# Optimization experiments

Measured on AMD Instinct MI355X. Metric: run time of the kernel, lower is better.

## Reference

```python
import jax, jax.numpy as jnp
import numpy as np

D_MODEL = 1024
HIDDEN = 4096
N_EXPERTS = 8
TOP_K = 2


def setup_inputs() -> dict:
    key = jax.random.key(0)
    ks = jax.random.split(key, 7)
    x = jax.random.normal(ks[0], (4, 2048, D_MODEL), dtype=jnp.float32)
    s = 0.02
    Wg = jax.random.normal(ks[1], (D_MODEL, N_EXPERTS), dtype=jnp.float32) * s
    bg = jnp.zeros((N_EXPERTS,), dtype=jnp.float32)
    W1 = jax.random.normal(ks[2], (N_EXPERTS, D_MODEL, HIDDEN), dtype=jnp.float32) * s
    b1 = jnp.zeros((N_EXPERTS, HIDDEN), dtype=jnp.float32)
    W2 = jax.random.normal(ks[3], (N_EXPERTS, HIDDEN, D_MODEL), dtype=jnp.float32) * s
    b2 = jnp.zeros((N_EXPERTS, D_MODEL), dtype=jnp.float32)
    return {"x": x, "Wg": Wg, "bg": bg, "W1": W1, "b1": b1, "W2": W2, "b2": b2}


def reference(x, Wg, bg, W1, b1, W2, b2):
    B, T, D = x.shape
    xf = x.reshape(-1, D)                      # (N, D)
    N = xf.shape[0]

    # --- top-k gate ---
    logits = xf @ Wg + bg                      # (N, E)
    all_probs = jax.nn.softmax(logits, axis=-1)
    topk_logits, topk_idx = jax.lax.top_k(logits, TOP_K)   # (N, k)
    topk_gates = jax.nn.softmax(topk_logits, axis=-1)      # (N, k), sums to 1

    # scatter gates into dense (N, E) masks (matches torch scatter_add_)
    rows = jnp.arange(N)[:, None]
    gate_mask = jnp.zeros((N, N_EXPERTS), dtype=xf.dtype).at[rows, topk_idx].add(topk_gates)
    dispatch_mask = jnp.zeros((N, N_EXPERTS), dtype=xf.dtype).at[rows, topk_idx].add(1.0)

    # --- experts: dense batched form; unselected tokens have gate 0 so math matches ---
    h = jnp.einsum('nd,edh->neh', xf, W1) + b1             # (N, E, H)
    h = jax.nn.relu(h)
    y = jnp.einsum('neh,ehd->ned', h, W2) + b2             # (N, E, D)
    out = jnp.einsum('ned,ne->nd', y, gate_mask)           # weighted combine
    outputs = out.reshape(B, T, D)

    # --- load-balance loss + metadata ---
    tokens_per_expert = (dispatch_mask > 0).sum(axis=0)
    assignment_fraction = gate_mask.sum(axis=0) / N
    expected_prob = all_probs.mean(axis=0)
    load_balance_loss = (expected_prob * assignment_fraction).sum() * N_EXPERTS

    return (outputs, load_balance_loss, tokens_per_expert, expected_prob, assignment_fraction)
```

## Files before the change

### kernel.cpp

```cpp
#include <hip/hip_runtime.h>
#include <stdint.h>

#define D_MODEL 1024
#define HID     4096
#define NE      8
#define NTOK    8192
#define NSLOT   (NTOK*2)
#define TM      128
#define MAX_RB  136
#define MPAD    (MAX_RB*TM)
#define HHALF   2048
#define GATE_BLOCKS 32

typedef unsigned short u16;
typedef __attribute__((ext_vector_type(8))) __bf16 bf16x8;
typedef __attribute__((ext_vector_type(4))) float  f32x4;

__device__ __forceinline__ u16 f2bu(float f){
  uint32_t u = __builtin_bit_cast(uint32_t, f);
  uint32_t r = (u + 0x7FFFu + ((u >> 16) & 1u)) >> 16;
  return (u16)r;
}

__device__ __forceinline__ void gload16(const u16* src, u16* lds){
  __builtin_amdgcn_global_load_lds((const __attribute__((address_space(1))) void*)src,
                                   (__attribute__((address_space(3))) void*)lds, 16, 0, 0);
}

__device__ __forceinline__ int xcd_swz(int w, int nwg){
  int q = nwg >> 3;
  return (w & 7) * q + (w >> 3);
}

#define WAITV(n) do{ asm volatile("s_waitcnt vmcnt(" #n ")" ::: "memory"); \
                     __builtin_amdgcn_sched_barrier(0); }while(0)
#define BARX()   do{ __builtin_amdgcn_sched_barrier(0); \
                     __builtin_amdgcn_s_barrier(); \
                     __builtin_amdgcn_sched_barrier(0); }while(0)

__global__ __launch_bounds__(256) void xcvt_kernel(const float* __restrict__ x, u16* __restrict__ x16){
  size_t i = (size_t)blockIdx.x*256 + threadIdx.x;
  const float4* p = (const float4*)(x + i*8);
  float4 a = p[0], b = p[1];
  u16 o[8] = {f2bu(a.x),f2bu(a.y),f2bu(a.z),f2bu(a.w),f2bu(b.x),f2bu(b.y),f2bu(b.z),f2bu(b.w)};
  *(int4*)(x16 + i*8) = *(int4*)o;
}

__global__ __launch_bounds__(256) void transpose_cvt(const float* __restrict__ in,
                                                     u16* __restrict__ out, int R, int C)
{
  __shared__ float tile[32][33];
  int e = blockIdx.z;
  int r0 = blockIdx.y * 32, c0 = blockIdx.x * 32;
  const float* src = in + (size_t)e * R * C;
  u16* dst = out + (size_t)e * R * C;
  int tx = threadIdx.x, ty = threadIdx.y;
#pragma unroll
  for (int i = 0; i < 4; i++){
    int r = r0 + ty + i*8;
    tile[ty + i*8][tx] = src[(size_t)r * C + c0 + tx];
  }
  __syncthreads();
#pragma unroll
  for (int i = 0; i < 4; i++){
    int c = c0 + ty + i*8;
    dst[(size_t)c * R + r0 + tx] = f2bu(tile[tx][ty + i*8]);
  }
}

__global__ __launch_bounds__(256) void gate_kernel(
    const float* __restrict__ x, const float* __restrict__ Wg, const float* __restrict__ bg,
    int* __restrict__ topk, float* __restrict__ gates,
    float* __restrict__ part_probs, float* __restrict__ part_assign, int* __restrict__ part_cnt)
{
  __shared__ float sp[256][8];
  __shared__ float sa[256][8];
  __shared__ int   sc[256][8];
  int t = threadIdx.x;
  int n = blockIdx.x * 256 + t;
  float lg[8];
#pragma unroll
  for (int e = 0; e < 8; e++) lg[e] = bg[e];
  const float4* xr = (const float4*)(x + (size_t)n * D_MODEL);
  for (int j = 0; j < D_MODEL/4; j++){
    float4 v = xr[j];
    const float* wr = Wg + (size_t)j * 32;
#pragma unroll
    for (int e = 0; e < 8; e++)
      lg[e] += v.x*wr[e] + v.y*wr[8+e] + v.z*wr[16+e] + v.w*wr[24+e];
  }
  float m = lg[0];
#pragma unroll
  for (int e = 1; e < 8; e++) m = fmaxf(m, lg[e]);
  float p[8]; float s = 0.f;
#pragma unroll
  for (int e = 0; e < 8; e++){ p[e] = expf(lg[e]-m); s += p[e]; }
  float inv = 1.f / s;
  int bi = 0; float best = lg[0];
#pragma unroll
  for (int e = 1; e < 8; e++) if (lg[e] > best){ best = lg[e]; bi = e; }
  int bi2 = 0; float best2 = -3.0e38f;
#pragma unroll
  for (int e = 0; e < 8; e++) if (e != bi && lg[e] > best2){ best2 = lg[e]; bi2 = e; }
  float t1 = expf(best2 - best);
  float g0 = 1.f / (1.f + t1);
  float g1 = t1 / (1.f + t1);
  topk[2*n] = bi;  topk[2*n+1] = bi2;
  gates[2*n] = g0; gates[2*n+1] = g1;
#pragma unroll
  for (int e = 0; e < 8; e++){
    sp[t][e] = p[e] * inv;
    sa[t][e] = (e == bi) ? g0 : ((e == bi2) ? g1 : 0.f);
    sc[t][e] = (e == bi || e == bi2) ? 1 : 0;
  }
  __syncthreads();
  if (t < 8){
    float s2 = 0.f; for (int i = 0; i < 256; i++) s2 += sp[i][t];
    part_probs[blockIdx.x*8 + t] = s2;
  } else if (t < 16){
    int e = t - 8; float s2 = 0.f; for (int i = 0; i < 256; i++) s2 += sa[i][e];
    part_assign[blockIdx.x*8 + e] = s2;
  } else if (t < 24){
    int e = t - 16; int c = 0; for (int i = 0; i < 256; i++) c += sc[i][e];
    part_cnt[blockIdx.x*8 + e] = c;
  }
}

__global__ __launch_bounds__(256) void scan_kernel(const int* __restrict__ part_cnt,
                                                   int* __restrict__ counts,
                                                   int* __restrict__ padded_off,
                                                   int* __restrict__ cursor,
                                                   int* __restrict__ block_expert,
                                                   int* __restrict__ routed)
{
  __shared__ int off[NE+1];
  int t = threadIdx.x;
  if (t == 0){
    int o = 0; off[0] = 0;
    for (int e = 0; e < NE; e++){
      int c = 0;
      for (int b = 0; b < GATE_BLOCKS; b++) c += part_cnt[b*8 + e];
      counts[e] = c;
      o += ((c + TM - 1) / TM) * TM;
      off[e+1] = o;
    }
    for (int e = 0; e <= NE; e++) padded_off[e] = off[e];
  }
  __syncthreads();
  if (t < NE) cursor[t] = 0;
  for (int rb = t; rb < MAX_RB; rb += 256){
    int e = -1;
    int r = rb * TM;
    for (int j = 0; j < NE; j++)
      if (r >= off[j] && r < off[j+1]) e = j;
    block_expert[rb] = e;
  }
  for (int i = t; i < MPAD; i += 256) routed[i] = -1;
}

__global__ __launch_bounds__(256) void place_kernel(const int* __restrict__ topk,
                                                    const int* __restrict__ padded_off,
                                                    int* __restrict__ cursor,
                                                    int* __restrict__ routed)
{
  int s = blockIdx.x * 256 + threadIdx.x;
  int e = topk[s];
  int pos = padded_off[e] + atomicAdd(&cursor[e], 1);
  routed[pos] = s;
}

__global__ __launch_bounds__(256, 3) void gemm1_kernel(
    const u16* __restrict__ x16, const u16* __restrict__ w1t, const float* __restrict__ b1,
    const int* __restrict__ routed, const int* __restrict__ block_expert,
    u16* __restrict__ h, int half)
{
  int l = xcd_swz(blockIdx.x, gridDim.x);
  int rb = l >> 4, cb = l & 15;
  int e = block_expert[rb];
  if (e < 0) return;
  __shared__ __align__(16) u16 Al[3][128][32];
  __shared__ __align__(16) u16 Bl[3][128][32];
  u16* AF = &Al[0][0][0];
  u16* BF = &Bl[0][0][0];
  int t = threadIdx.x;
  int lane = t & 63, wid = t >> 6;

  int srow0 = wid*32 + (lane >> 2);
  int sch = (lane & 3) * 8;

  int slot0 = routed[rb*TM + srow0];
  int slot1 = routed[rb*TM + srow0 + 16];
  int tok0 = slot0 >= 0 ? (slot0 >> 1) : 0;
  int tok1 = slot1 >= 0 ? (slot1 >> 1) : 0;
  const u16* srcA0 = x16 + (size_t)tok0 * D_MODEL + sch;
  const u16* srcA1 = x16 + (size_t)tok1 * D_MODEL + sch;
  const u16* wb = w1t + ((size_t)e*HID + (size_t)half*HHALF + (size_t)cb*128) * D_MODEL + sch;
  const u16* srcB0 = wb + (size_t)srow0 * D_MODEL;
  const u16* srcB1 = wb + (size_t)(srow0 + 16) * D_MODEL;

  int wr = wid >> 1, wc = wid & 1;
  int fr = lane & 15, fk = lane >> 4;
  f32x4 acc[4][4];
#pragma unroll
  for (int i = 0; i < 4; i++)
#pragma unroll
    for (int j = 0; j < 4; j++) acc[i][j] = (f32x4){0.f,0.f,0.f,0.f};

#define STG1(bo, kk) do{ \
    gload16(srcA0 + (kk), AF + (bo) + wid*1024); \
    gload16(srcA1 + (kk), AF + (bo) + wid*1024 + 512); \
    gload16(srcB0 + (kk), BF + (bo) + wid*1024); \
    gload16(srcB1 + (kk), BF + (bo) + wid*1024 + 512); } while(0)

#define CMP1(bo) do{ \
    bf16x8 af[4], bf[4]; \
    _Pragma("unroll") \
    for (int mm = 0; mm < 4; mm++) af[mm] = *(const bf16x8*)(AF + (bo) + (wr*64 + mm*16 + fr)*32 + fk*8); \
    _Pragma("unroll") \
    for (int nn = 0; nn < 4; nn++) bf[nn] = *(const bf16x8*)(BF + (bo) + (wc*64 + nn*16 + fr)*32 + fk*8); \
    _Pragma("unroll") \
    for (int mm = 0; mm < 4; mm++) \
      _Pragma("unroll") \
      for (int nn = 0; nn < 4; nn++) \
        acc[mm][nn] = __builtin_amdgcn_mfma_f32_16x16x32_bf16(af[mm], bf[nn], acc[mm][nn], 0, 0, 0); } while(0)

  const int nk = D_MODEL/32;
  STG1(0, 0); STG1(4096, 32); STG1(8192, 64);
  int bo = 0;
  for (int i = 0; i < nk - 2; i++){
    WAITV(8);
    BARX();
    CMP1(bo);
    BARX();
    if (i < nk - 3) STG1(bo, (i+3)*32);
    bo = (bo == 8192) ? 0 : bo + 4096;
  }
  WAITV(4); BARX(); CMP1(bo); BARX();
  bo = (bo == 8192) ? 0 : bo + 4096;
  WAITV(0); BARX(); CMP1(bo);

  int r4 = fk * 4;
#pragma unroll
  for (int nn = 0; nn < 4; nn++){
    int ct = wc*64 + nn*16 + fr;
    float bias = b1[(size_t)e*HID + (size_t)half*HHALF + cb*128 + ct];
#pragma unroll
    for (int mm = 0; mm < 4; mm++){
#pragma unroll
      for (int r = 0; r < 4; r++){
        int rt = wr*64 + mm*16 + r4 + r;
        float v = acc[mm][nn][r] + bias;
        v = v > 0.f ? v : 0.f;
        h[(size_t)(rb*TM + rt) * HHALF + cb*128 + ct] = f2bu(v);
      }
    }
  }
#undef STG1
#undef CMP1
}

__global__ __launch_bounds__(256, 3) void gemm2_kernel(
    const u16* __restrict__ h, const u16* __restrict__ w2t,
    const int* __restrict__ routed, const int* __restrict__ block_expert,
    const float* __restrict__ gates, float* __restrict__ y, int half)
{
  int l = xcd_swz(blockIdx.x, gridDim.x);
  int rb = l >> 3, cb = l & 7;
  int e = block_expert[rb];
  if (e < 0) return;
  __shared__ __align__(16) u16 Al[3][128][32];
  __shared__ __align__(16) u16 Bl[3][128][32];
  __shared__ int   rslot[128];
  __shared__ float rgate[128];
  u16* AF = &Al[0][0][0];
  u16* BF = &Bl[0][0][0];
  int t = threadIdx.x;
  int lane = t & 63, wid = t >> 6;
  if (t < 128){
    int s = routed[rb*TM + t];
    rslot[t] = s;
    rgate[t] = (s >= 0) ? gates[s] : 0.f;
  }

  int srow0 = wid*32 + (lane >> 2);
  int sch = (lane & 3) * 8;
  const u16* srcA0 = h + (size_t)(rb*TM + srow0) * HHALF + sch;
  const u16* srcA1 = h + (size_t)(rb*TM + srow0 + 16) * HHALF + sch;
  const u16* wb = w2t + ((size_t)e*D_MODEL + (size_t)cb*128) * HID + (size_t)half*HHALF + sch;
  const u16* srcB0 = wb + (size_t)srow0 * HID;
  const u16* srcB1 = wb + (size_t)(srow0 + 16) * HID;

  int wr = wid >> 1, wc = wid & 1;
  int fr = lane & 15, fk = lane >> 4;
  f32x4 acc[4][4];
#pragma unroll
  for (int i = 0; i < 4; i++)
#pragma unroll
    for (int j = 0; j < 4; j++) acc[i][j] = (f32x4){0.f,0.f,0.f,0.f};

#define STG2(bo, kk) do{ \
    gload16(srcA0 + (kk), AF + (bo) + wid*1024); \
    gload16(srcA1 + (kk), AF + (bo) + wid*1024 + 512); \
    gload16(srcB0 + (kk), BF + (bo) + wid*1024); \
    gload16(srcB1 + (kk), BF + (bo) + wid*1024 + 512); } while(0)

#define CMP2(bo) do{ \
    bf16x8 af[4], bf[4]; \
    _Pragma("unroll") \
    for (int mm = 0; mm < 4; mm++) af[mm] = *(const bf16x8*)(AF + (bo) + (wr*64 + mm*16 + fr)*32 + fk*8); \
    _Pragma("unroll") \
    for (int nn = 0; nn < 4; nn++) bf[nn] = *(const bf16x8*)(BF + (bo) + (wc*64 + nn*16 + fr)*32 + fk*8); \
    _Pragma("unroll") \
    for (int mm = 0; mm < 4; mm++) \
      _Pragma("unroll") \
      for (int nn = 0; nn < 4; nn++) \
        acc[mm][nn] = __builtin_amdgcn_mfma_f32_16x16x32_bf16(af[mm], bf[nn], acc[mm][nn], 0, 0, 0); } while(0)

  const int nk = HHALF/32;
  STG2(0, 0); STG2(4096, 32); STG2(8192, 64);
  int bo = 0;
  for (int i = 0; i < nk - 2; i++){
    WAITV(8);
    BARX();
    CMP2(bo);
    BARX();
    if (i < nk - 3) STG2(bo, (i+3)*32);
    bo = (bo == 8192) ? 0 : bo + 4096;
  }
  WAITV(4); BARX(); CMP2(bo); BARX();
  bo = (bo == 8192) ? 0 : bo + 4096;
  WAITV(0); BARX(); CMP2(bo);

  int r4 = fk * 4;
#pragma unroll
  for (int mm = 0; mm < 4; mm++){
#pragma unroll
    for (int r = 0; r < 4; r++){
      int rt = wr*64 + mm*16 + r4 + r;
      int slot = rslot[rt];
      if (slot < 0) continue;
      float g = rgate[rt];
#pragma unroll
      for (int nn = 0; nn < 4; nn++){
        int ct = wc*64 + nn*16 + fr;
        size_t idx = (size_t)slot * D_MODEL + cb*128 + ct;
        float val = g * acc[mm][nn][r];
        if (half == 0) y[idx] = val;
        else           y[idx] += val;
      }
    }
  }
#undef STG2
#undef CMP2
}

__global__ __launch_bounds__(256) void combine_kernel(
    const float* __restrict__ y, const int* __restrict__ topk, const float* __restrict__ gates,
    const float* __restrict__ b2, float* __restrict__ out)
{
  int i = blockIdx.x * 256 + threadIdx.x;
  int n = i >> 8;
  int d = (i & 255) * 4;
  float4 a  = *(const float4*)(y + (size_t)(2*n)   * D_MODEL + d);
  float4 b  = *(const float4*)(y + (size_t)(2*n+1) * D_MODEL + d);
  int e0 = topk[2*n], e1 = topk[2*n+1];
  float g0 = gates[2*n], g1 = gates[2*n+1];
  float4 c0 = *(const float4*)(b2 + (size_t)e0 * D_MODEL + d);
  float4 c1 = *(const float4*)(b2 + (size_t)e1 * D_MODEL + d);
  float4 o;
  o.x = a.x + b.x + g0*c0.x + g1*c1.x;
  o.y = a.y + b.y + g0*c0.y + g1*c1.y;
  o.z = a.z + b.z + g0*c0.z + g1*c1.z;
  o.w = a.w + b.w + g0*c0.w + g1*c1.w;
  *(float4*)(out + (size_t)n * D_MODEL + d) = o;
}

__global__ void finalize_kernel(const float* __restrict__ part_probs,
                                const float* __restrict__ part_assign,
                                const int* __restrict__ counts,
                                float* __restrict__ out_tail)
{
  __shared__ float ep[8], af[8];
  int t = threadIdx.x;
  if (t < 8){
    float s = 0.f;
    for (int b = 0; b < GATE_BLOCKS; b++) s += part_probs[b*8 + t];
    ep[t] = s / (float)NTOK;
  } else if (t < 16){
    int e = t - 8; float s = 0.f;
    for (int b = 0; b < GATE_BLOCKS; b++) s += part_assign[b*8 + e];
    af[e] = s / (float)NTOK;
  }
  __syncthreads();
  if (t == 0){
    float loss = 0.f;
    for (int e = 0; e < 8; e++) loss += ep[e] * af[e];
    out_tail[0] = loss * (float)NE;
  }
  if (t < 8){
    out_tail[1 + t]  = (float)counts[t];
    out_tail[9 + t]  = ep[t];
    out_tail[17 + t] = af[t];
  }
}

extern "C" void kernel_launch(void* const* d_in, const int* in_sizes, int n_in,
                              void* d_out, int out_size, void* d_ws, size_t ws_size,
                              hipStream_t stream)
{
  const float* x  = (const float*)d_in[0];
  const float* Wg = (const float*)d_in[1];
  const float* bg = (const float*)d_in[2];
  const float* W1 = (const float*)d_in[3];
  const float* b1 = (const float*)d_in[4];
  const float* W2 = (const float*)d_in[5];
  const float* b2 = (const float*)d_in[6];
  float* out = (float*)d_out;

  char* ws = (char*)d_ws;
  size_t o = 0;
  auto alloc = [&](size_t bytes) -> char* {
    char* p = ws + o; o = (o + bytes + 255) & ~(size_t)255; return p;
  };
  int*   topk        = (int*)   alloc((size_t)NSLOT*4);
  float* gates       = (float*) alloc((size_t)NSLOT*4);
  int*   counts      = (int*)   alloc(NE*4);
  int*   padded_off  = (int*)   alloc((NE+1)*4);
  int*   cursor      = (int*)   alloc(NE*4);
  int*   block_exp   = (int*)   alloc(MAX_RB*4);
  int*   routed      = (int*)   alloc((size_t)MPAD*4);
  float* part_probs  = (float*) alloc(GATE_BLOCKS*8*4);
  float* part_assign = (float*) alloc(GATE_BLOCKS*8*4);
  int*   part_cnt    = (int*)   alloc(GATE_BLOCKS*8*4);
  u16*   x16         = (u16*)   alloc((size_t)NTOK*D_MODEL*2);
  u16*   w1t         = (u16*)   alloc((size_t)NE*HID*D_MODEL*2);
  u16*   w2t         = (u16*)   alloc((size_t)NE*HID*D_MODEL*2);
  u16*   hbuf        = (u16*)   alloc((size_t)MPAD*HHALF*2);
  float* ybuf        = (float*) alloc((size_t)NSLOT*D_MODEL*4);
  (void)ws_size; (void)in_sizes; (void)n_in; (void)out_size;

  transpose_cvt<<<dim3(HID/32, D_MODEL/32, NE), dim3(32,8), 0, stream>>>(W1, w1t, D_MODEL, HID);
  transpose_cvt<<<dim3(D_MODEL/32, HID/32, NE), dim3(32,8), 0, stream>>>(W2, w2t, HID, D_MODEL);
  xcvt_kernel<<<(NTOK*D_MODEL)/(256*8), 256, 0, stream>>>(x, x16);
  gate_kernel<<<GATE_BLOCKS, 256, 0, stream>>>(x, Wg, bg, topk, gates, part_probs, part_assign, part_cnt);
  scan_kernel<<<1, 256, 0, stream>>>(part_cnt, counts, padded_off, cursor, block_exp, routed);
  place_kernel<<<NSLOT/256, 256, 0, stream>>>(topk, padded_off, cursor, routed);
  for (int half = 0; half < 2; half++){
    gemm1_kernel<<<16*MAX_RB, 256, 0, stream>>>(x16, w1t, b1, routed, block_exp, hbuf, half);
    gemm2_kernel<<<8*MAX_RB, 256, 0, stream>>>(hbuf, w2t, routed, block_exp, gates, ybuf, half);
  }
  combine_kernel<<<NTOK, 256, 0, stream>>>(ybuf, topk, gates, b2, out);
  finalize_kernel<<<1, 64, 0, stream>>>(part_probs, part_assign, counts, out + (size_t)NTOK*D_MODEL);
}
```

Before: 688.4 us.

## Enlarge expert GEMM tiles to 256x256 with 512-thread blocks

Doubles the GEMM block tile from 128x128 to 256x256, uses 8 waves per block, and raises the routing row-block size to 256, so MAX_RB and the grid shapes change to match. Each wave now computes 128x64 and loads its A fragments one at a time. The aim is more data reuse per LDS load and less global traffic per flop. In exchange, the larger row blocks add more padding waste per expert, the grids are smaller with possible tail imbalance, and the bigger accumulators raise register pressure (launch bounds 512,2) with 96KB of LDS per block.

```diff
diff --git a/kernel.cpp b/kernel.cpp
--- a/kernel.cpp
+++ b/kernel.cpp
@@ -6,8 +6,8 @@
 #define NE      8
 #define NTOK    8192
 #define NSLOT   (NTOK*2)
-#define TM      128
-#define MAX_RB  136
+#define TM      256
+#define MAX_RB  72
 #define MPAD    (MAX_RB*TM)
 #define HHALF   2048
 #define GATE_BLOCKS 32
@@ -169,63 +169,64 @@
   routed[pos] = s;
 }
 
-__global__ __launch_bounds__(256, 3) void gemm1_kernel(
+
+__global__ __launch_bounds__(512, 2) void gemm1_kernel(
     const u16* __restrict__ x16, const u16* __restrict__ w1t, const float* __restrict__ b1,
     const int* __restrict__ routed, const int* __restrict__ block_expert,
     u16* __restrict__ h, int half)
 {
   int l = xcd_swz(blockIdx.x, gridDim.x);
-  int rb = l >> 4, cb = l & 15;
+  int rb = l >> 3, cb = l & 7;
   int e = block_expert[rb];
   if (e < 0) return;
-  __shared__ __align__(16) u16 Al[3][128][32];
-  __shared__ __align__(16) u16 Bl[3][128][32];
+  __shared__ __align__(16) u16 Al[3][256][32];
+  __shared__ __align__(16) u16 Bl[3][256][32];
   u16* AF = &Al[0][0][0];
   u16* BF = &Bl[0][0][0];
   int t = threadIdx.x;
   int lane = t & 63, wid = t >> 6;
 
-  int srow0 = wid*32 + (lane >> 2);
+  int srow = wid*16 + (lane >> 2);
   int sch = (lane & 3) * 8;
 
-  int slot0 = routed[rb*TM + srow0];
-  int slot1 = routed[rb*TM + srow0 + 16];
+  int slot0 = routed[rb*TM + srow];
+  int slot1 = routed[rb*TM + srow + 128];
   int tok0 = slot0 >= 0 ? (slot0 >> 1) : 0;
   int tok1 = slot1 >= 0 ? (slot1 >> 1) : 0;
   const u16* srcA0 = x16 + (size_t)tok0 * D_MODEL + sch;
   const u16* srcA1 = x16 + (size_t)tok1 * D_MODEL + sch;
-  const u16* wb = w1t + ((size_t)e*HID + (size_t)half*HHALF + (size_t)cb*128) * D_MODEL + sch;
-  const u16* srcB0 = wb + (size_t)srow0 * D_MODEL;
-  const u16* srcB1 = wb + (size_t)(srow0 + 16) * D_MODEL;
-
-  int wr = wid >> 1, wc = wid & 1;
+  const u16* wb = w1t + ((size_t)e*HID + (size_t)half*HHALF + (size_t)cb*256) * D_MODEL + sch;
+  const u16* srcB0 = wb + (size_t)srow * D_MODEL;
+  const u16* srcB1 = wb + (size_t)(srow + 128) * D_MODEL;
+
+  int wr = wid >> 2, wc = wid & 3;
   int fr = lane & 15, fk = lane >> 4;
-  f32x4 acc[4][4];
-#pragma unroll
-  for (int i = 0; i < 4; i++)
+  f32x4 acc[8][4];
+#pragma unroll
+  for (int i = 0; i < 8; i++)
 #pragma unroll
     for (int j = 0; j < 4; j++) acc[i][j] = (f32x4){0.f,0.f,0.f,0.f};
 
 #define STG1(bo, kk) do{ \
-    gload16(srcA0 + (kk), AF + (bo) + wid*1024); \
-    gload16(srcA1 + (kk), AF + (bo) + wid*1024 + 512); \
-    gload16(srcB0 + (kk), BF + (bo) + wid*1024); \
-    gload16(srcB1 + (kk), BF + (bo) + wid*1024 + 512); } while(0)
+    gload16(srcA0 + (kk), AF + (bo) + wid*512); \
+    gload16(srcA1 + (kk), AF + (bo) + wid*512 + 4096); \
+    gload16(srcB0 + (kk), BF + (bo) + wid*512); \
+    gload16(srcB1 + (kk), BF + (bo) + wid*512 + 4096); } while(0)
 
 #define CMP1(bo) do{ \
-    bf16x8 af[4], bf[4]; \
+    bf16x8 bfr[4]; \
     _Pragma("unroll") \
-    for (int mm = 0; mm < 4; mm++) af[mm] = *(const bf16x8*)(AF + (bo) + (wr*64 + mm*16 + fr)*32 + fk*8); \
+    for (int nn = 0; nn < 4; nn++) bfr[nn] = *(const bf16x8*)(BF + (bo) + (wc*64 + nn*16 + fr)*32 + fk*8); \
     _Pragma("unroll") \
-    for (int nn = 0; nn < 4; nn++) bf[nn] = *(const bf16x8*)(BF + (bo) + (wc*64 + nn*16 + fr)*32 + fk*8); \
-    _Pragma("unroll") \
-    for (int mm = 0; mm < 4; mm++) \
+    for (int mm = 0; mm < 8; mm++){ \
+      bf16x8 af = *(const bf16x8*)(AF + (bo) + (wr*128 + mm*16 + fr)*32 + fk*8); \
       _Pragma("unroll") \
       for (int nn = 0; nn < 4; nn++) \
-        acc[mm][nn] = __builtin_amdgcn_mfma_f32_16x16x32_bf16(af[mm], bf[nn], acc[mm][nn], 0, 0, 0); } while(0)
+        acc[mm][nn] = __builtin_amdgcn_mfma_f32_16x16x32_bf16(af, bfr[nn], acc[mm][nn], 0, 0, 0); \
+    } } while(0)
 
   const int nk = D_MODEL/32;
-  STG1(0, 0); STG1(4096, 32); STG1(8192, 64);
+  STG1(0, 0); STG1(8192, 32); STG1(16384, 64);
   int bo = 0;
   for (int i = 0; i < nk - 2; i++){
     WAITV(8);
@@ -233,25 +234,25 @@
     CMP1(bo);
     BARX();
     if (i < nk - 3) STG1(bo, (i+3)*32);
-    bo = (bo == 8192) ? 0 : bo + 4096;
+    bo = (bo == 16384) ? 0 : bo + 8192;
   }
   WAITV(4); BARX(); CMP1(bo); BARX();
-  bo = (bo == 8192) ? 0 : bo + 4096;
+  bo = (bo == 16384) ? 0 : bo + 8192;
   WAITV(0); BARX(); CMP1(bo);
 
   int r4 = fk * 4;
 #pragma unroll
   for (int nn = 0; nn < 4; nn++){
     int ct = wc*64 + nn*16 + fr;
-    float bias = b1[(size_t)e*HID + (size_t)half*HHALF + cb*128 + ct];
-#pragma unroll
-    for (int mm = 0; mm < 4; mm++){
+    float bias = b1[(size_t)e*HID + (size_t)half*HHALF + cb*256 + ct];
+#pragma unroll
+    for (int mm = 0; mm < 8; mm++){
 #pragma unroll
       for (int r = 0; r < 4; r++){
-        int rt = wr*64 + mm*16 + r4 + r;
+        int rt = wr*128 + mm*16 + r4 + r;
         float v = acc[mm][nn][r] + bias;
         v = v > 0.f ? v : 0.f;
-        h[(size_t)(rb*TM + rt) * HHALF + cb*128 + ct] = f2bu(v);
+        h[(size_t)(rb*TM + rt) * HHALF + cb*256 + ct] = f2bu(v);
       }
     }
   }
@@ -259,65 +260,65 @@
 #undef CMP1
 }
 
-__global__ __launch_bounds__(256, 3) void gemm2_kernel(
+__global__ __launch_bounds__(512, 2) void gemm2_kernel(
     const u16* __restrict__ h, const u16* __restrict__ w2t,
     const int* __restrict__ routed, const int* __restrict__ block_expert,
     const float* __restrict__ gates, float* __restrict__ y, int half)
 {
   int l = xcd_swz(blockIdx.x, gridDim.x);
-  int rb = l >> 3, cb = l & 7;
+  int rb = l >> 2, cb = l & 3;
   int e = block_expert[rb];
   if (e < 0) return;
-  __shared__ __align__(16) u16 Al[3][128][32];
-  __shared__ __align__(16) u16 Bl[3][128][32];
-  __shared__ int   rslot[128];
-  __shared__ float rgate[128];
+  __shared__ __align__(16) u16 Al[3][256][32];
+  __shared__ __align__(16) u16 Bl[3][256][32];
+  __shared__ int   rslot[256];
+  __shared__ float rgate[256];
   u16* AF = &Al[0][0][0];
   u16* BF = &Bl[0][0][0];
   int t = threadIdx.x;
   int lane = t & 63, wid = t >> 6;
-  if (t < 128){
+  if (t < 256){
     int s = routed[rb*TM + t];
     rslot[t] = s;
     rgate[t] = (s >= 0) ? gates[s] : 0.f;
   }
 
-  int srow0 = wid*32 + (lane >> 2);
+  int srow = wid*16 + (lane >> 2);
   int sch = (lane & 3) * 8;
-  const u16* srcA0 = h + (size_t)(rb*TM + srow0) * HHALF + sch;
-  const u16* srcA1 = h + (size_t)(rb*TM + srow0 + 16) * HHALF + sch;
-  const u16* wb = w2t + ((size_t)e*D_MODEL + (size_t)cb*128) * HID + (size_t)half*HHALF + sch;
-  const u16* srcB0 = wb + (size_t)srow0 * HID;
-  const u16* srcB1 = wb + (size_t)(srow0 + 16) * HID;
-
-  int wr = wid >> 1, wc = wid & 1;
+  const u16* srcA0 = h + (size_t)(rb*TM + srow) * HHALF + sch;
+  const u16* srcA1 = h + (size_t)(rb*TM + srow + 128) * HHALF + sch;
+  const u16* wb = w2t + ((size_t)e*D_MODEL + (size_t)cb*256) * HID + (size_t)half*HHALF + sch;
+  const u16* srcB0 = wb + (size_t)srow * HID;
+  const u16* srcB1 = wb + (size_t)(srow + 128) * HID;
+
+  int wr = wid >> 2, wc = wid & 3;
   int fr = lane & 15, fk = lane >> 4;
-  f32x4 acc[4][4];
-#pragma unroll
-  for (int i = 0; i < 4; i++)
+  f32x4 acc[8][4];
+#pragma unroll
+  for (int i = 0; i < 8; i++)
 #pragma unroll
     for (int j = 0; j < 4; j++) acc[i][j] = (f32x4){0.f,0.f,0.f,0.f};
 
 #define STG2(bo, kk) do{ \
-    gload16(srcA0 + (kk), AF + (bo) + wid*1024); \
-    gload16(srcA1 + (kk), AF + (bo) + wid*1024 + 512); \
-    gload16(srcB0 + (kk), BF + (bo) + wid*1024); \
-    gload16(srcB1 + (kk), BF + (bo) + wid*1024 + 512); } while(0)
+    gload16(srcA0 + (kk), AF + (bo) + wid*512); \
+    gload16(srcA1 + (kk), AF + (bo) + wid*512 + 4096); \
+    gload16(srcB0 + (kk), BF + (bo) + wid*512); \
+    gload16(srcB1 + (kk), BF + (bo) + wid*512 + 4096); } while(0)
 
 #define CMP2(bo) do{ \
-    bf16x8 af[4], bf[4]; \
+    bf16x8 bfr[4]; \
     _Pragma("unroll") \
-    for (int mm = 0; mm < 4; mm++) af[mm] = *(const bf16x8*)(AF + (bo) + (wr*64 + mm*16 + fr)*32 + fk*8); \
+    for (int nn = 0; nn < 4; nn++) bfr[nn] = *(const bf16x8*)(BF + (bo) + (wc*64 + nn*16 + fr)*32 + fk*8); \
     _Pragma("unroll") \
-    for (int nn = 0; nn < 4; nn++) bf[nn] = *(const bf16x8*)(BF + (bo) + (wc*64 + nn*16 + fr)*32 + fk*8); \
-    _Pragma("unroll") \
-    for (int mm = 0; mm < 4; mm++) \
+    for (int mm = 0; mm < 8; mm++){ \
+      bf16x8 af = *(const bf16x8*)(AF + (bo) + (wr*128 + mm*16 + fr)*32 + fk*8); \
       _Pragma("unroll") \
       for (int nn = 0; nn < 4; nn++) \
-        acc[mm][nn] = __builtin_amdgcn_mfma_f32_16x16x32_bf16(af[mm], bf[nn], acc[mm][nn], 0, 0, 0); } while(0)
+        acc[mm][nn] = __builtin_amdgcn_mfma_f32_16x16x32_bf16(af, bfr[nn], acc[mm][nn], 0, 0, 0); \
+    } } while(0)
 
   const int nk = HHALF/32;
-  STG2(0, 0); STG2(4096, 32); STG2(8192, 64);
+  STG2(0, 0); STG2(8192, 32); STG2(16384, 64);
   int bo = 0;
   for (int i = 0; i < nk - 2; i++){
     WAITV(8);
@@ -325,25 +326,25 @@
     CMP2(bo);
     BARX();
     if (i < nk - 3) STG2(bo, (i+3)*32);
-    bo = (bo == 8192) ? 0 : bo + 4096;
+    bo = (bo == 16384) ? 0 : bo + 8192;
   }
   WAITV(4); BARX(); CMP2(bo); BARX();
-  bo = (bo == 8192) ? 0 : bo + 4096;
+  bo = (bo == 16384) ? 0 : bo + 8192;
   WAITV(0); BARX(); CMP2(bo);
 
   int r4 = fk * 4;
 #pragma unroll
-  for (int mm = 0; mm < 4; mm++){
+  for (int mm = 0; mm < 8; mm++){
 #pragma unroll
     for (int r = 0; r < 4; r++){
-      int rt = wr*64 + mm*16 + r4 + r;
+      int rt = wr*128 + mm*16 + r4 + r;
       int slot = rslot[rt];
       if (slot < 0) continue;
       float g = rgate[rt];
 #pragma unroll
       for (int nn = 0; nn < 4; nn++){
         int ct = wc*64 + nn*16 + fr;
-        size_t idx = (size_t)slot * D_MODEL + cb*128 + ct;
+        size_t idx = (size_t)slot * D_MODEL + cb*256 + ct;
         float val = g * acc[mm][nn][r];
         if (half == 0) y[idx] = val;
         else           y[idx] += val;
@@ -446,8 +447,8 @@
   scan_kernel<<<1, 256, 0, stream>>>(part_cnt, counts, padded_off, cursor, block_exp, routed);
   place_kernel<<<NSLOT/256, 256, 0, stream>>>(topk, padded_off, cursor, routed);
   for (int half = 0; half < 2; half++){
-    gemm1_kernel<<<16*MAX_RB, 256, 0, stream>>>(x16, w1t, b1, routed, block_exp, hbuf, half);
-    gemm2_kernel<<<8*MAX_RB, 256, 0, stream>>>(hbuf, w2t, routed, block_exp, gates, ybuf, half);
+    gemm1_kernel<<<8*MAX_RB, 512, 0, stream>>>(x16, w1t, b1, routed, block_exp, hbuf, half);
+    gemm2_kernel<<<4*MAX_RB, 512, 0, stream>>>(hbuf, w2t, routed, block_exp, gates, ybuf, half);
   }
   combine_kernel<<<NTOK, 256, 0, stream>>>(ybuf, topk, gates, b2, out);
   finalize_kernel<<<1, 64, 0, stream>>>(part_probs, part_assign, counts, out + (size_t)NTOK*D_MODEL);
```

Result: slower. 927.5 us (+34.7%).
